# Optimization experiments

Hardware: AMD Instinct MI355X
Metric: run time of the kernel (lower is better)

Reference implementation:

```python
import jax, jax.numpy as jnp
import numpy as np

HEADS = 8
H_DIM = 64
SCALE = H_DIM ** -0.5


def setup_inputs() -> dict:
    key = jax.random.key(0)
    ks = jax.random.split(key, 10)
    B, Q, K, D = 4, 2048, 2048, 512
    hidden = HEADS * H_DIM  # 512
    s = 0.02  # weight init scale
    return {
        "q": jax.random.normal(ks[0], (B, Q, D), jnp.float32),
        "k": jax.random.normal(ks[1], (B, K, D), jnp.float32),
        "v": jax.random.normal(ks[2], (B, K, D), jnp.float32),
        "bias": jax.random.normal(ks[3], (B, Q, K), jnp.float32),
        "Wq": jax.random.normal(ks[4], (D, hidden), jnp.float32) * s,
        "bq": jnp.zeros((hidden,), jnp.float32),
        "Wk": jax.random.normal(ks[5], (D, hidden), jnp.float32) * s,
        "bk": jnp.zeros((hidden,), jnp.float32),
        "Wv": jax.random.normal(ks[6], (D, hidden), jnp.float32) * s,
        "bv": jnp.zeros((hidden,), jnp.float32),
        "Wg": jax.random.normal(ks[7], (D, hidden), jnp.float32) * s,
        "bg": jnp.zeros((hidden,), jnp.float32),
        "Wo": jax.random.normal(ks[8], (hidden, D), jnp.float32) * s,
        "bo": jnp.zeros((D,), jnp.float32),
    }


def reference(q, k, v, bias, Wq, bq, Wk, bk, Wv, bv, Wg, bg, Wo, bo):
    B, Q, _ = q.shape
    K = k.shape[-2]
    wq = (q @ Wq + bq).reshape(B, Q, HEADS, H_DIM) * SCALE   # (B,Q,H,Dh)
    wk = (k @ Wk + bk).reshape(B, K, HEADS, H_DIM)           # (B,K,H,Dh)
    wv = (v @ Wv + bv).reshape(B, K, HEADS, H_DIM)           # (B,K,H,Dh)
    # scores (B,Q,K,H); softmax over k_len axis (-2), matching torch softmax(-2)
    scores = jnp.einsum("bqhd,bkhd->bqkh", wq, wk)
    a = jax.nn.softmax(scores, axis=-2)
    # bias added AFTER softmax, broadcast over heads -- faithful to source
    a = a + bias[..., None]
    o = jnp.einsum("bqkh,bkhd->bqhd", a, wv).reshape(B, Q, HEADS * H_DIM)
    g = jax.nn.sigmoid(q @ Wg + bg)
    o = g * o
    return o @ Wo + bo
```

## Files before the change

### kernel.cpp

```cpp
#include <hip/hip_runtime.h>
#include <hip/hip_bf16.h>

#define NB 4
#define SEQ 2048
#define DMODEL 512
#define HEADS 8
#define HDIM 64
#define QKSCALE 0.125f

typedef __bf16 bf16_t;
typedef bf16_t bf16x8 __attribute__((ext_vector_type(8)));
typedef bf16_t bf16x4 __attribute__((ext_vector_type(4)));
typedef float f32x4 __attribute__((ext_vector_type(4)));

__device__ __forceinline__ int swz(int row, int c16) {
    return (row << 7) + (((c16) ^ (row & 7)) << 4);
}

__device__ __forceinline__ bf16x4 cvt4(float4 v) {
    bf16x4 r;
    r[0] = (bf16_t)v.x; r[1] = (bf16_t)v.y; r[2] = (bf16_t)v.z; r[3] = (bf16_t)v.w;
    return r;
}

__global__ __launch_bounds__(256) void prep_weights(
    const float* __restrict__ Wq, const float* __restrict__ Wk,
    const float* __restrict__ Wv, const float* __restrict__ Wg,
    const float* __restrict__ Wo, bf16_t* __restrict__ out)
{
    __shared__ float t[64][65];
    const int m  = blockIdx.x >> 6;
    const int t2 = blockIdx.x & 63;
    const int tr = t2 >> 3, tc = t2 & 7;
    const float* W = (m == 0) ? Wq : (m == 1) ? Wk : (m == 2) ? Wv : (m == 3) ? Wg : Wo;
    const int r0 = threadIdx.x >> 6;
    const int c  = threadIdx.x & 63;
#pragma unroll
    for (int i = 0; i < 64; i += 4) {
        int row = i + r0;
        t[row][c] = W[(size_t)(tr * 64 + row) * DMODEL + tc * 64 + c];
    }
    __syncthreads();
    bf16_t* o = out + (size_t)m * (DMODEL * DMODEL);
#pragma unroll
    for (int i = 0; i < 64; i += 4) {
        int row = i + r0;
        o[(size_t)(tc * 64 + row) * DMODEL + tr * 64 + c] = (bf16_t)t[c][row];
    }
}

template <int MODE>
__global__ __launch_bounds__(256) void gemm_proj(
    const float* __restrict__ A, const bf16_t* __restrict__ Wt,
    const float* __restrict__ bias, void* __restrict__ out, float scale)
{
    __shared__ __align__(16) char smA[8192];
    __shared__ __align__(16) char smB[8192];
    const int tid = threadIdx.x;
    const int lane = tid & 63, w = tid >> 6;
    const int m0 = (blockIdx.x >> 3) << 6;
    const int n0 = (blockIdx.x & 7) << 6;
    const int wrow = (w >> 1) * 32, wcol = (w & 1) * 32;
    const int lr = lane & 15, lg = lane >> 4;

    f32x4 acc[2][2] = {};
    for (int kb = 0; kb < 8; ++kb) {
        const int k0 = kb * 64;
        __syncthreads();
#pragma unroll
        for (int i = 0; i < 4; ++i) {
            int f = tid + i * 256;
            int row = f >> 4, c4 = f & 15;
            float4 v = *(const float4*)(A + (size_t)(m0 + row) * DMODEL + k0 + c4 * 4);
            *(bf16x4*)(smA + swz(row, c4 >> 1) + ((c4 & 1) << 3)) = cvt4(v);
        }
#pragma unroll
        for (int i = 0; i < 2; ++i) {
            int f = tid + i * 256;
            int row = f >> 3, c16 = f & 7;
            uint4 v = *(const uint4*)(Wt + (size_t)(n0 + row) * DMODEL + k0 + c16 * 8);
            *(uint4*)(smB + swz(row, c16)) = v;
        }
        __syncthreads();
#pragma unroll
        for (int ks = 0; ks < 2; ++ks) {
            bf16x8 a[2], b[2];
#pragma unroll
            for (int mi = 0; mi < 2; ++mi)
                a[mi] = *(const bf16x8*)(smA + swz(wrow + mi * 16 + lr, lg + ks * 4));
#pragma unroll
            for (int ni = 0; ni < 2; ++ni)
                b[ni] = *(const bf16x8*)(smB + swz(wcol + ni * 16 + lr, lg + ks * 4));
#pragma unroll
            for (int mi = 0; mi < 2; ++mi)
#pragma unroll
                for (int ni = 0; ni < 2; ++ni)
                    acc[mi][ni] = __builtin_amdgcn_mfma_f32_16x16x32_bf16(a[mi], b[ni], acc[mi][ni], 0, 0, 0);
        }
    }
#pragma unroll
    for (int mi = 0; mi < 2; ++mi) {
#pragma unroll
        for (int ni = 0; ni < 2; ++ni) {
            const int col = n0 + wcol + ni * 16 + lr;
            const float bv = bias[col];
            if (MODE == 0) {
#pragma unroll
                for (int j = 0; j < 4; ++j) {
                    int row = m0 + wrow + mi * 16 + (lg << 2) + j;
                    ((bf16_t*)out)[(size_t)row * DMODEL + col] = (bf16_t)((acc[mi][ni][j] + bv) * scale);
                }
            } else if (MODE == 1) {
                int row0 = m0 + wrow + mi * 16 + (lg << 2);
                int b = row0 >> 11, key = row0 & (SEQ - 1);
                int h = col >> 6, d = col & 63;
                bf16x4 r;
#pragma unroll
                for (int j = 0; j < 4; ++j) r[j] = (bf16_t)(acc[mi][ni][j] + bv);
                *(bf16x4*)((bf16_t*)out + ((size_t)(b * HEADS + h) * HDIM + d) * SEQ + key) = r;
            } else {
#pragma unroll
                for (int j = 0; j < 4; ++j) {
                    int row = m0 + wrow + mi * 16 + (lg << 2) + j;
                    float x = acc[mi][ni][j] + bv;
                    ((bf16_t*)out)[(size_t)row * DMODEL + col] = (bf16_t)(1.0f / (1.0f + __expf(-x)));
                }
            }
        }
    }
}

__global__ __launch_bounds__(256) void attn_kernel(
    const bf16_t* __restrict__ wq, const bf16_t* __restrict__ wk,
    const bf16_t* __restrict__ wvt, bf16_t* __restrict__ attn_o)
{
    __shared__ __align__(16) char smK[8192];
    __shared__ __align__(16) char smV[8192];
    __shared__ __align__(16) char smP[8192];
    const int tid = threadIdx.x;
    const int lane = tid & 63, w = tid >> 6;
    const int bh = blockIdx.x & 31;
    const int qt = blockIdx.x >> 5;
    const int b = bh >> 3, h = bh & 7;
    const int q0 = qt << 6;
    const int lr = lane & 15, lg = lane >> 4;

    bf16x8 qf[2];
    {
        int row = q0 + w * 16 + lr;
        const bf16_t* p = wq + (size_t)(b * SEQ + row) * DMODEL + h * HDIM + lg * 8;
        qf[0] = *(const bf16x8*)(p);
        qf[1] = *(const bf16x8*)(p + 32);
    }
    float mrun[4], lrun[4];
#pragma unroll
    for (int j = 0; j < 4; ++j) { mrun[j] = -1e30f; lrun[j] = 0.f; }
    f32x4 oacc[4] = {};

    for (int kt = 0; kt < SEQ / 64; ++kt) {
        const int k0 = kt * 64;
        __syncthreads();
#pragma unroll
        for (int i = 0; i < 2; ++i) {
            int f = tid + i * 256;
            int row = f >> 3, c16 = f & 7;
            uint4 vk = *(const uint4*)(wk + (size_t)(b * SEQ + k0 + row) * DMODEL + h * HDIM + c16 * 8);
            *(uint4*)(smK + swz(row, c16)) = vk;
            uint4 vv = *(const uint4*)(wvt + ((size_t)(b * HEADS + h) * HDIM + row) * SEQ + k0 + c16 * 8);
            *(uint4*)(smV + swz(row, c16)) = vv;
        }
        __syncthreads();

        f32x4 s[4] = {};
#pragma unroll
        for (int ks = 0; ks < 2; ++ks) {
#pragma unroll
            for (int nf = 0; nf < 4; ++nf) {
                bf16x8 kbf = *(const bf16x8*)(smK + swz(nf * 16 + lr, lg + ks * 4));
                s[nf] = __builtin_amdgcn_mfma_f32_16x16x32_bf16(qf[ks], kbf, s[nf], 0, 0, 0);
            }
        }
        float mnew[4], sc[4], rs[4];
#pragma unroll
        for (int j = 0; j < 4; ++j) {
            float m = fmaxf(fmaxf(s[0][j], s[1][j]), fmaxf(s[2][j], s[3][j]));
#pragma unroll
            for (int off = 1; off < 16; off <<= 1) m = fmaxf(m, __shfl_xor(m, off));
            mnew[j] = fmaxf(mrun[j], m);
            sc[j] = __expf(mrun[j] - mnew[j]);
            rs[j] = 0.f;
        }
#pragma unroll
        for (int nf = 0; nf < 4; ++nf) {
#pragma unroll
            for (int j = 0; j < 4; ++j) {
                float p = __expf(s[nf][j] - mnew[j]);
                s[nf][j] = p;
                rs[j] += p;
            }
        }
#pragma unroll
        for (int j = 0; j < 4; ++j) {
#pragma unroll
            for (int off = 1; off < 16; off <<= 1) rs[j] += __shfl_xor(rs[j], off);
            lrun[j] = lrun[j] * sc[j] + rs[j];
            mrun[j] = mnew[j];
        }
#pragma unroll
        for (int nf = 0; nf < 4; ++nf)
#pragma unroll
            for (int j = 0; j < 4; ++j) oacc[nf][j] *= sc[j];

        char* pbase = smP + w * 2048;
#pragma unroll
        for (int nf = 0; nf < 4; ++nf) {
            int col = nf * 16 + lr;
#pragma unroll
            for (int j = 0; j < 4; ++j) {
                int row = lg * 4 + j;
                *(bf16_t*)(pbase + swz(row, col >> 3) + ((col & 7) << 1)) = (bf16_t)s[nf][j];
            }
        }
#pragma unroll
        for (int ks = 0; ks < 2; ++ks) {
            bf16x8 pa = *(const bf16x8*)(pbase + swz(lr, lg + ks * 4));
#pragma unroll
            for (int nf = 0; nf < 4; ++nf) {
                bf16x8 vb = *(const bf16x8*)(smV + swz(nf * 16 + lr, lg + ks * 4));
                oacc[nf] = __builtin_amdgcn_mfma_f32_16x16x32_bf16(pa, vb, oacc[nf], 0, 0, 0);
            }
        }
    }
    float rinv[4];
#pragma unroll
    for (int j = 0; j < 4; ++j) rinv[j] = 1.0f / lrun[j];
#pragma unroll
    for (int nf = 0; nf < 4; ++nf) {
        int col = h * HDIM + nf * 16 + lr;
#pragma unroll
        for (int j = 0; j < 4; ++j) {
            int row = q0 + w * 16 + lg * 4 + j;
            attn_o[(size_t)(b * SEQ + row) * DMODEL + col] = (bf16_t)(oacc[nf][j] * rinv[j]);
        }
    }
}

__global__ __launch_bounds__(512) void biasv_gemm(
    const float* __restrict__ bias, const bf16_t* __restrict__ wvt,
    float* __restrict__ Bv)
{
    __shared__ __align__(16) char smA[16384];
    __shared__ __align__(16) char smB[16384];
    const int tid = threadIdx.x;
    const int lane = tid & 63, w = tid >> 6;
    const int nt = blockIdx.x & 3;
    const int mt = (blockIdx.x >> 2) & 15;
    const int b = blockIdx.x >> 6;
    const int m0 = mt << 7, n0 = nt << 7;
    const int wr = w >> 2, wc = w & 3;
    const int lr = lane & 15, lg = lane >> 4;

    f32x4 acc[4][2] = {};
    for (int kb = 0; kb < SEQ / 64; ++kb) {
        const int k0 = kb * 64;
        __syncthreads();
#pragma unroll
        for (int i = 0; i < 4; ++i) {
            int f = tid + i * 512;
            int row = f >> 4, c4 = f & 15;
            float4 v = *(const float4*)(bias + ((size_t)b * SEQ + m0 + row) * SEQ + k0 + c4 * 4);
            *(bf16x4*)(smA + swz(row, c4 >> 1) + ((c4 & 1) << 3)) = cvt4(v);
        }
#pragma unroll
        for (int i = 0; i < 2; ++i) {
            int f = tid + i * 512;
            int row = f >> 3, c16 = f & 7;
            int n = n0 + row;
            uint4 v = *(const uint4*)(wvt + ((size_t)(b * HEADS + (n >> 6)) * HDIM + (n & 63)) * SEQ + k0 + c16 * 8);
            *(uint4*)(smB + swz(row, c16)) = v;
        }
        __syncthreads();
#pragma unroll
        for (int ks = 0; ks < 2; ++ks) {
            bf16x8 a[4], bb[2];
#pragma unroll
            for (int mi = 0; mi < 4; ++mi)
                a[mi] = *(const bf16x8*)(smA + swz(wr * 64 + mi * 16 + lr, lg + ks * 4));
#pragma unroll
            for (int ni = 0; ni < 2; ++ni)
                bb[ni] = *(const bf16x8*)(smB + swz(wc * 32 + ni * 16 + lr, lg + ks * 4));
#pragma unroll
            for (int mi = 0; mi < 4; ++mi)
#pragma unroll
                for (int ni = 0; ni < 2; ++ni)
                    acc[mi][ni] = __builtin_amdgcn_mfma_f32_16x16x32_bf16(a[mi], bb[ni], acc[mi][ni], 0, 0, 0);
        }
    }
#pragma unroll
    for (int mi = 0; mi < 4; ++mi) {
#pragma unroll
        for (int ni = 0; ni < 2; ++ni) {
            int col = n0 + wc * 32 + ni * 16 + lr;
#pragma unroll
            for (int j = 0; j < 4; ++j) {
                int row = m0 + wr * 64 + mi * 16 + lg * 4 + j;
                Bv[((size_t)b * SEQ + row) * DMODEL + col] = acc[mi][ni][j];
            }
        }
    }
}

__global__ __launch_bounds__(256) void out_gemm(
    const bf16_t* __restrict__ atn, const float* __restrict__ Bvp,
    const bf16_t* __restrict__ gg, const bf16_t* __restrict__ Wot,
    const float* __restrict__ bo, float* __restrict__ out)
{
    __shared__ __align__(16) char smA[8192];
    __shared__ __align__(16) char smB[8192];
    const int tid = threadIdx.x;
    const int lane = tid & 63, w = tid >> 6;
    const int m0 = (blockIdx.x >> 3) << 6;
    const int n0 = (blockIdx.x & 7) << 6;
    const int wrow = (w >> 1) * 32, wcol = (w & 1) * 32;
    const int lr = lane & 15, lg = lane >> 4;

    f32x4 acc[2][2] = {};
    for (int kb = 0; kb < 8; ++kb) {
        const int k0 = kb * 64;
        __syncthreads();
#pragma unroll
        for (int i = 0; i < 4; ++i) {
            int f = tid + i * 256;
            int row = f >> 4, c4 = f & 15;
            size_t idx = (size_t)(m0 + row) * DMODEL + k0 + c4 * 4;
            bf16x4 a4 = *(const bf16x4*)(atn + idx);
            bf16x4 g4 = *(const bf16x4*)(gg + idx);
            float4 b4 = *(const float4*)(Bvp + idx);
            bf16x4 r;
            r[0] = (bf16_t)((float)g4[0] * ((float)a4[0] + b4.x));
            r[1] = (bf16_t)((float)g4[1] * ((float)a4[1] + b4.y));
            r[2] = (bf16_t)((float)g4[2] * ((float)a4[2] + b4.z));
            r[3] = (bf16_t)((float)g4[3] * ((float)a4[3] + b4.w));
            *(bf16x4*)(smA + swz(row, c4 >> 1) + ((c4 & 1) << 3)) = r;
        }
#pragma unroll
        for (int i = 0; i < 2; ++i) {
            int f = tid + i * 256;
            int row = f >> 3, c16 = f & 7;
            uint4 v = *(const uint4*)(Wot + (size_t)(n0 + row) * DMODEL + k0 + c16 * 8);
            *(uint4*)(smB + swz(row, c16)) = v;
        }
        __syncthreads();
#pragma unroll
        for (int ks = 0; ks < 2; ++ks) {
            bf16x8 a[2], b[2];
#pragma unroll
            for (int mi = 0; mi < 2; ++mi)
                a[mi] = *(const bf16x8*)(smA + swz(wrow + mi * 16 + lr, lg + ks * 4));
#pragma unroll
            for (int ni = 0; ni < 2; ++ni)
                b[ni] = *(const bf16x8*)(smB + swz(wcol + ni * 16 + lr, lg + ks * 4));
#pragma unroll
            for (int mi = 0; mi < 2; ++mi)
#pragma unroll
                for (int ni = 0; ni < 2; ++ni)
                    acc[mi][ni] = __builtin_amdgcn_mfma_f32_16x16x32_bf16(a[mi], b[ni], acc[mi][ni], 0, 0, 0);
        }
    }
#pragma unroll
    for (int mi = 0; mi < 2; ++mi) {
#pragma unroll
        for (int ni = 0; ni < 2; ++ni) {
            int col = n0 + wcol + ni * 16 + lr;
            float bb = bo[col];
#pragma unroll
            for (int j = 0; j < 4; ++j) {
                int row = m0 + wrow + mi * 16 + (lg << 2) + j;
                out[(size_t)row * DMODEL + col] = acc[mi][ni][j] + bb;
            }
        }
    }
}

extern "C" void kernel_launch(void* const* d_in, const int* in_sizes, int n_in,
                              void* d_out, int out_size, void* d_ws, size_t ws_size,
                              hipStream_t stream)
{
    const float* q    = (const float*)d_in[0];
    const float* k    = (const float*)d_in[1];
    const float* v    = (const float*)d_in[2];
    const float* bias = (const float*)d_in[3];
    const float* Wq   = (const float*)d_in[4];
    const float* bq   = (const float*)d_in[5];
    const float* Wk   = (const float*)d_in[6];
    const float* bk   = (const float*)d_in[7];
    const float* Wv   = (const float*)d_in[8];
    const float* bv   = (const float*)d_in[9];
    const float* Wg   = (const float*)d_in[10];
    const float* bg   = (const float*)d_in[11];
    const float* Wo   = (const float*)d_in[12];
    const float* bo   = (const float*)d_in[13];
    float* out = (float*)d_out;

    char* ws = (char*)d_ws;
    const size_t WSZ = (size_t)DMODEL * DMODEL;
    const size_t TOK = (size_t)NB * SEQ * DMODEL;
    bf16_t* Wt   = (bf16_t*)ws;
    bf16_t* wq_  = (bf16_t*)(ws + 5 * WSZ * 2);
    bf16_t* wk_  = wq_ + TOK;
    bf16_t* wvt  = wk_ + TOK;
    bf16_t* atn  = wvt + TOK;
    bf16_t* g_   = atn + TOK;
    float*  Bv_  = (float*)(g_ + TOK);

    prep_weights<<<320, 256, 0, stream>>>(Wq, Wk, Wv, Wg, Wo, Wt);
    gemm_proj<0><<<1024, 256, 0, stream>>>(q, Wt,            bq, (void*)wq_, QKSCALE);
    gemm_proj<0><<<1024, 256, 0, stream>>>(k, Wt + WSZ,      bk, (void*)wk_, 1.0f);
    gemm_proj<1><<<1024, 256, 0, stream>>>(v, Wt + 2 * WSZ,  bv, (void*)wvt, 1.0f);
    gemm_proj<2><<<1024, 256, 0, stream>>>(q, Wt + 3 * WSZ,  bg, (void*)g_,  1.0f);
    attn_kernel<<<1024, 256, 0, stream>>>(wq_, wk_, wvt, atn);
    biasv_gemm<<<256, 512, 0, stream>>>(bias, wvt, Bv_);
    out_gemm<<<1024, 256, 0, stream>>>(atn, Bv_, g_, Wt + 4 * WSZ, bo, out);
}
```

Measured before the change: 481.4 us.

## Fuse Q/gate projections, enlarge GEMM tiles, prefetch K/V, drop softmax max tracking

The Q and gate projections become one GEMM with N=1024 by reordering the transposed weights, which removes a duplicate pass over q. The projection and output GEMMs move to 128x128 tiles with 512 threads, and the output GEMM staging loads are widened to 8 elements. The attention loop prefetches the next K/V tile into registers while it computes on the current one. The online softmax max and rescale are removed in favour of exp2 with log2(e) folded into the Q scale, so the row sum is only reduced at the end. That last change depends on the scores staying small enough that exp does not overflow.

```diff
diff --git a/kernel.cpp b/kernel.cpp
--- a/kernel.cpp
+++ b/kernel.cpp
@@ -6,7 +6,7 @@
 #define DMODEL 512
 #define HEADS 8
 #define HDIM 64
-#define QKSCALE 0.125f
+#define QKS_L2E 0.18033688011112042f
 
 typedef __bf16 bf16_t;
 typedef bf16_t bf16x8 __attribute__((ext_vector_type(8)));
@@ -24,15 +24,15 @@
 }
 
 __global__ __launch_bounds__(256) void prep_weights(
-    const float* __restrict__ Wq, const float* __restrict__ Wk,
-    const float* __restrict__ Wv, const float* __restrict__ Wg,
+    const float* __restrict__ Wq, const float* __restrict__ Wg,
+    const float* __restrict__ Wk, const float* __restrict__ Wv,
     const float* __restrict__ Wo, bf16_t* __restrict__ out)
 {
     __shared__ float t[64][65];
     const int m  = blockIdx.x >> 6;
     const int t2 = blockIdx.x & 63;
     const int tr = t2 >> 3, tc = t2 & 7;
-    const float* W = (m == 0) ? Wq : (m == 1) ? Wk : (m == 2) ? Wv : (m == 3) ? Wg : Wo;
+    const float* W = (m == 0) ? Wq : (m == 1) ? Wg : (m == 2) ? Wk : (m == 3) ? Wv : Wo;
     const int r0 = threadIdx.x >> 6;
     const int c  = threadIdx.x & 63;
 #pragma unroll
@@ -50,33 +50,36 @@
 }
 
 template <int MODE>
-__global__ __launch_bounds__(256) void gemm_proj(
+__global__ __launch_bounds__(512) void proj_gemm(
     const float* __restrict__ A, const bf16_t* __restrict__ Wt,
-    const float* __restrict__ bias, void* __restrict__ out, float scale)
-{
-    __shared__ __align__(16) char smA[8192];
-    __shared__ __align__(16) char smB[8192];
+    const float* __restrict__ bias0, const float* __restrict__ bias1,
+    bf16_t* __restrict__ out0, bf16_t* __restrict__ out1)
+{
+    constexpr int NT = (MODE == 0) ? 8 : 4;
+    __shared__ __align__(16) char smA[16384];
+    __shared__ __align__(16) char smB[16384];
     const int tid = threadIdx.x;
     const int lane = tid & 63, w = tid >> 6;
-    const int m0 = (blockIdx.x >> 3) << 6;
-    const int n0 = (blockIdx.x & 7) << 6;
-    const int wrow = (w >> 1) * 32, wcol = (w & 1) * 32;
+    const int nt = blockIdx.x & (NT - 1);
+    const int mt = blockIdx.x / NT;
+    const int m0 = mt << 7, n0 = nt << 7;
+    const int wr = w >> 2, wc = w & 3;
     const int lr = lane & 15, lg = lane >> 4;
 
-    f32x4 acc[2][2] = {};
+    f32x4 acc[4][2] = {};
     for (int kb = 0; kb < 8; ++kb) {
         const int k0 = kb * 64;
         __syncthreads();
 #pragma unroll
         for (int i = 0; i < 4; ++i) {
-            int f = tid + i * 256;
+            int f = tid + i * 512;
             int row = f >> 4, c4 = f & 15;
             float4 v = *(const float4*)(A + (size_t)(m0 + row) * DMODEL + k0 + c4 * 4);
             *(bf16x4*)(smA + swz(row, c4 >> 1) + ((c4 & 1) << 3)) = cvt4(v);
         }
 #pragma unroll
         for (int i = 0; i < 2; ++i) {
-            int f = tid + i * 256;
+            int f = tid + i * 512;
             int row = f >> 3, c16 = f & 7;
             uint4 v = *(const uint4*)(Wt + (size_t)(n0 + row) * DMODEL + k0 + c16 * 8);
             *(uint4*)(smB + swz(row, c16)) = v;
@@ -84,47 +87,50 @@
         __syncthreads();
 #pragma unroll
         for (int ks = 0; ks < 2; ++ks) {
-            bf16x8 a[2], b[2];
-#pragma unroll
-            for (int mi = 0; mi < 2; ++mi)
-                a[mi] = *(const bf16x8*)(smA + swz(wrow + mi * 16 + lr, lg + ks * 4));
+            bf16x8 a[4], bb[2];
+#pragma unroll
+            for (int mi = 0; mi < 4; ++mi)
+                a[mi] = *(const bf16x8*)(smA + swz(wr * 64 + mi * 16 + lr, lg + ks * 4));
 #pragma unroll
             for (int ni = 0; ni < 2; ++ni)
-                b[ni] = *(const bf16x8*)(smB + swz(wcol + ni * 16 + lr, lg + ks * 4));
-#pragma unroll
-            for (int mi = 0; mi < 2; ++mi)
+                bb[ni] = *(const bf16x8*)(smB + swz(wc * 32 + ni * 16 + lr, lg + ks * 4));
+#pragma unroll
+            for (int mi = 0; mi < 4; ++mi)
 #pragma unroll
                 for (int ni = 0; ni < 2; ++ni)
-                    acc[mi][ni] = __builtin_amdgcn_mfma_f32_16x16x32_bf16(a[mi], b[ni], acc[mi][ni], 0, 0, 0);
-        }
-    }
-#pragma unroll
-    for (int mi = 0; mi < 2; ++mi) {
+                    acc[mi][ni] = __builtin_amdgcn_mfma_f32_16x16x32_bf16(a[mi], bb[ni], acc[mi][ni], 0, 0, 0);
+        }
+    }
+#pragma unroll
+    for (int mi = 0; mi < 4; ++mi) {
 #pragma unroll
         for (int ni = 0; ni < 2; ++ni) {
-            const int col = n0 + wcol + ni * 16 + lr;
-            const float bv = bias[col];
+            const int col = n0 + wc * 32 + ni * 16 + lr;
+            const int row0 = m0 + wr * 64 + mi * 16 + lg * 4;
             if (MODE == 0) {
+                const bool isG = col >= DMODEL;
+                const int c = isG ? col - DMODEL : col;
+                const float bb = isG ? bias1[c] : bias0[c];
 #pragma unroll
                 for (int j = 0; j < 4; ++j) {
-                    int row = m0 + wrow + mi * 16 + (lg << 2) + j;
-                    ((bf16_t*)out)[(size_t)row * DMODEL + col] = (bf16_t)((acc[mi][ni][j] + bv) * scale);
+                    float x = acc[mi][ni][j] + bb;
+                    bf16_t r = isG ? (bf16_t)(1.0f / (1.0f + __expf(-x)))
+                                   : (bf16_t)(x * QKS_L2E);
+                    (isG ? out1 : out0)[(size_t)(row0 + j) * DMODEL + c] = r;
                 }
             } else if (MODE == 1) {
-                int row0 = m0 + wrow + mi * 16 + (lg << 2);
-                int b = row0 >> 11, key = row0 & (SEQ - 1);
-                int h = col >> 6, d = col & 63;
+                const float bb = bias0[col];
+#pragma unroll
+                for (int j = 0; j < 4; ++j)
+                    out0[(size_t)(row0 + j) * DMODEL + col] = (bf16_t)(acc[mi][ni][j] + bb);
+            } else {
+                const float bb = bias0[col];
+                const int b = row0 >> 11, key = row0 & (SEQ - 1);
+                const int h = col >> 6, d = col & 63;
                 bf16x4 r;
 #pragma unroll
-                for (int j = 0; j < 4; ++j) r[j] = (bf16_t)(acc[mi][ni][j] + bv);
-                *(bf16x4*)((bf16_t*)out + ((size_t)(b * HEADS + h) * HDIM + d) * SEQ + key) = r;
-            } else {
-#pragma unroll
-                for (int j = 0; j < 4; ++j) {
-                    int row = m0 + wrow + mi * 16 + (lg << 2) + j;
-                    float x = acc[mi][ni][j] + bv;
-                    ((bf16_t*)out)[(size_t)row * DMODEL + col] = (bf16_t)(1.0f / (1.0f + __expf(-x)));
-                }
+                for (int j = 0; j < 4; ++j) r[j] = (bf16_t)(acc[mi][ni][j] + bb);
+                *(bf16x4*)(out0 + ((size_t)(b * HEADS + h) * HDIM + d) * SEQ + key) = r;
             }
         }
     }
@@ -152,24 +158,34 @@
         qf[0] = *(const bf16x8*)(p);
         qf[1] = *(const bf16x8*)(p + 32);
     }
-    float mrun[4], lrun[4];
-#pragma unroll
-    for (int j = 0; j < 4; ++j) { mrun[j] = -1e30f; lrun[j] = 0.f; }
+    const bf16_t* kbase = wk + (size_t)b * SEQ * DMODEL + h * HDIM;
+    const bf16_t* vbase = wvt + (size_t)(b * HEADS + h) * HDIM * SEQ;
+    const int srow0 = tid >> 3,        sc0 = tid & 7;
+    const int srow1 = (tid + 256) >> 3, sc1 = (tid + 256) & 7;
+
+    uint4 rk[2], rv[2];
+    rk[0] = *(const uint4*)(kbase + (size_t)srow0 * DMODEL + sc0 * 8);
+    rk[1] = *(const uint4*)(kbase + (size_t)srow1 * DMODEL + sc1 * 8);
+    rv[0] = *(const uint4*)(vbase + (size_t)srow0 * SEQ + sc0 * 8);
+    rv[1] = *(const uint4*)(vbase + (size_t)srow1 * SEQ + sc1 * 8);
+
+    float lsum[4] = {0.f, 0.f, 0.f, 0.f};
     f32x4 oacc[4] = {};
 
     for (int kt = 0; kt < SEQ / 64; ++kt) {
-        const int k0 = kt * 64;
-        __syncthreads();
-#pragma unroll
-        for (int i = 0; i < 2; ++i) {
-            int f = tid + i * 256;
-            int row = f >> 3, c16 = f & 7;
-            uint4 vk = *(const uint4*)(wk + (size_t)(b * SEQ + k0 + row) * DMODEL + h * HDIM + c16 * 8);
-            *(uint4*)(smK + swz(row, c16)) = vk;
-            uint4 vv = *(const uint4*)(wvt + ((size_t)(b * HEADS + h) * HDIM + row) * SEQ + k0 + c16 * 8);
-            *(uint4*)(smV + swz(row, c16)) = vv;
-        }
-        __syncthreads();
+        __syncthreads();
+        *(uint4*)(smK + swz(srow0, sc0)) = rk[0];
+        *(uint4*)(smK + swz(srow1, sc1)) = rk[1];
+        *(uint4*)(smV + swz(srow0, sc0)) = rv[0];
+        *(uint4*)(smV + swz(srow1, sc1)) = rv[1];
+        __syncthreads();
+        if (kt + 1 < SEQ / 64) {
+            const int k0n = (kt + 1) * 64;
+            rk[0] = *(const uint4*)(kbase + (size_t)(k0n + srow0) * DMODEL + sc0 * 8);
+            rk[1] = *(const uint4*)(kbase + (size_t)(k0n + srow1) * DMODEL + sc1 * 8);
+            rv[0] = *(const uint4*)(vbase + (size_t)srow0 * SEQ + k0n + sc0 * 8);
+            rv[1] = *(const uint4*)(vbase + (size_t)srow1 * SEQ + k0n + sc1 * 8);
+        }
 
         f32x4 s[4] = {};
 #pragma unroll
@@ -180,37 +196,15 @@
                 s[nf] = __builtin_amdgcn_mfma_f32_16x16x32_bf16(qf[ks], kbf, s[nf], 0, 0, 0);
             }
         }
-        float mnew[4], sc[4], rs[4];
-#pragma unroll
-        for (int j = 0; j < 4; ++j) {
-            float m = fmaxf(fmaxf(s[0][j], s[1][j]), fmaxf(s[2][j], s[3][j]));
-#pragma unroll
-            for (int off = 1; off < 16; off <<= 1) m = fmaxf(m, __shfl_xor(m, off));
-            mnew[j] = fmaxf(mrun[j], m);
-            sc[j] = __expf(mrun[j] - mnew[j]);
-            rs[j] = 0.f;
-        }
 #pragma unroll
         for (int nf = 0; nf < 4; ++nf) {
 #pragma unroll
             for (int j = 0; j < 4; ++j) {
-                float p = __expf(s[nf][j] - mnew[j]);
+                float p = __builtin_amdgcn_exp2f(s[nf][j]);
                 s[nf][j] = p;
-                rs[j] += p;
-            }
-        }
-#pragma unroll
-        for (int j = 0; j < 4; ++j) {
-#pragma unroll
-            for (int off = 1; off < 16; off <<= 1) rs[j] += __shfl_xor(rs[j], off);
-            lrun[j] = lrun[j] * sc[j] + rs[j];
-            mrun[j] = mnew[j];
-        }
-#pragma unroll
-        for (int nf = 0; nf < 4; ++nf)
-#pragma unroll
-            for (int j = 0; j < 4; ++j) oacc[nf][j] *= sc[j];
-
+                lsum[j] += p;
+            }
+        }
         char* pbase = smP + w * 2048;
 #pragma unroll
         for (int nf = 0; nf < 4; ++nf) {
@@ -233,7 +227,12 @@
     }
     float rinv[4];
 #pragma unroll
-    for (int j = 0; j < 4; ++j) rinv[j] = 1.0f / lrun[j];
+    for (int j = 0; j < 4; ++j) {
+        float t = lsum[j];
+#pragma unroll
+        for (int off = 1; off < 16; off <<= 1) t += __shfl_xor(t, off);
+        rinv[j] = 1.0f / t;
+    }
 #pragma unroll
     for (int nf = 0; nf < 4; ++nf) {
         int col = h * HDIM + nf * 16 + lr;
@@ -310,42 +309,48 @@
     }
 }
 
-__global__ __launch_bounds__(256) void out_gemm(
+__global__ __launch_bounds__(512) void out_gemm(
     const bf16_t* __restrict__ atn, const float* __restrict__ Bvp,
     const bf16_t* __restrict__ gg, const bf16_t* __restrict__ Wot,
     const float* __restrict__ bo, float* __restrict__ out)
 {
-    __shared__ __align__(16) char smA[8192];
-    __shared__ __align__(16) char smB[8192];
+    __shared__ __align__(16) char smA[16384];
+    __shared__ __align__(16) char smB[16384];
     const int tid = threadIdx.x;
     const int lane = tid & 63, w = tid >> 6;
-    const int m0 = (blockIdx.x >> 3) << 6;
-    const int n0 = (blockIdx.x & 7) << 6;
-    const int wrow = (w >> 1) * 32, wcol = (w & 1) * 32;
+    const int nt = blockIdx.x & 3;
+    const int mt = blockIdx.x >> 2;
+    const int m0 = mt << 7, n0 = nt << 7;
+    const int wr = w >> 2, wc = w & 3;
     const int lr = lane & 15, lg = lane >> 4;
 
-    f32x4 acc[2][2] = {};
+    f32x4 acc[4][2] = {};
     for (int kb = 0; kb < 8; ++kb) {
         const int k0 = kb * 64;
         __syncthreads();
 #pragma unroll
-        for (int i = 0; i < 4; ++i) {
-            int f = tid + i * 256;
-            int row = f >> 4, c4 = f & 15;
-            size_t idx = (size_t)(m0 + row) * DMODEL + k0 + c4 * 4;
-            bf16x4 a4 = *(const bf16x4*)(atn + idx);
-            bf16x4 g4 = *(const bf16x4*)(gg + idx);
-            float4 b4 = *(const float4*)(Bvp + idx);
-            bf16x4 r;
-            r[0] = (bf16_t)((float)g4[0] * ((float)a4[0] + b4.x));
-            r[1] = (bf16_t)((float)g4[1] * ((float)a4[1] + b4.y));
-            r[2] = (bf16_t)((float)g4[2] * ((float)a4[2] + b4.z));
-            r[3] = (bf16_t)((float)g4[3] * ((float)a4[3] + b4.w));
-            *(bf16x4*)(smA + swz(row, c4 >> 1) + ((c4 & 1) << 3)) = r;
-        }
-#pragma unroll
         for (int i = 0; i < 2; ++i) {
-            int f = tid + i * 256;
+            int f = tid + i * 512;
+            int row = f >> 3, c8 = f & 7;
+            size_t idx = (size_t)(m0 + row) * DMODEL + k0 + c8 * 8;
+            bf16x8 a8 = *(const bf16x8*)(atn + idx);
+            bf16x8 g8 = *(const bf16x8*)(gg + idx);
+            float4 blo = *(const float4*)(Bvp + idx);
+            float4 bhi = *(const float4*)(Bvp + idx + 4);
+            bf16x8 r;
+            r[0] = (bf16_t)((float)g8[0] * ((float)a8[0] + blo.x));
+            r[1] = (bf16_t)((float)g8[1] * ((float)a8[1] + blo.y));
+            r[2] = (bf16_t)((float)g8[2] * ((float)a8[2] + blo.z));
+            r[3] = (bf16_t)((float)g8[3] * ((float)a8[3] + blo.w));
+            r[4] = (bf16_t)((float)g8[4] * ((float)a8[4] + bhi.x));
+            r[5] = (bf16_t)((float)g8[5] * ((float)a8[5] + bhi.y));
+            r[6] = (bf16_t)((float)g8[6] * ((float)a8[6] + bhi.z));
+            r[7] = (bf16_t)((float)g8[7] * ((float)a8[7] + bhi.w));
+            *(bf16x8*)(smA + swz(row, c8)) = r;
+        }
+#pragma unroll
+        for (int i = 0; i < 2; ++i) {
+            int f = tid + i * 512;
             int row = f >> 3, c16 = f & 7;
             uint4 v = *(const uint4*)(Wot + (size_t)(n0 + row) * DMODEL + k0 + c16 * 8);
             *(uint4*)(smB + swz(row, c16)) = v;
@@ -353,29 +358,29 @@
         __syncthreads();
 #pragma unroll
         for (int ks = 0; ks < 2; ++ks) {
-            bf16x8 a[2], b[2];
-#pragma unroll
-            for (int mi = 0; mi < 2; ++mi)
-                a[mi] = *(const bf16x8*)(smA + swz(wrow + mi * 16 + lr, lg + ks * 4));
+            bf16x8 a[4], bb[2];
+#pragma unroll
+            for (int mi = 0; mi < 4; ++mi)
+                a[mi] = *(const bf16x8*)(smA + swz(wr * 64 + mi * 16 + lr, lg + ks * 4));
 #pragma unroll
             for (int ni = 0; ni < 2; ++ni)
-                b[ni] = *(const bf16x8*)(smB + swz(wcol + ni * 16 + lr, lg + ks * 4));
-#pragma unroll
-            for (int mi = 0; mi < 2; ++mi)
+                bb[ni] = *(const bf16x8*)(smB + swz(wc * 32 + ni * 16 + lr, lg + ks * 4));
+#pragma unroll
+            for (int mi = 0; mi < 4; ++mi)
 #pragma unroll
                 for (int ni = 0; ni < 2; ++ni)
-                    acc[mi][ni] = __builtin_amdgcn_mfma_f32_16x16x32_bf16(a[mi], b[ni], acc[mi][ni], 0, 0, 0);
-        }
-    }
-#pragma unroll
-    for (int mi = 0; mi < 2; ++mi) {
+                    acc[mi][ni] = __builtin_amdgcn_mfma_f32_16x16x32_bf16(a[mi], bb[ni], acc[mi][ni], 0, 0, 0);
+        }
+    }
+#pragma unroll
+    for (int mi = 0; mi < 4; ++mi) {
 #pragma unroll
         for (int ni = 0; ni < 2; ++ni) {
-            int col = n0 + wcol + ni * 16 + lr;
+            int col = n0 + wc * 32 + ni * 16 + lr;
             float bb = bo[col];
 #pragma unroll
             for (int j = 0; j < 4; ++j) {
-                int row = m0 + wrow + mi * 16 + (lg << 2) + j;
+                int row = m0 + wr * 64 + mi * 16 + lg * 4 + j;
                 out[(size_t)row * DMODEL + col] = acc[mi][ni][j] + bb;
             }
         }
@@ -413,12 +418,11 @@
     bf16_t* g_   = atn + TOK;
     float*  Bv_  = (float*)(g_ + TOK);
 
-    prep_weights<<<320, 256, 0, stream>>>(Wq, Wk, Wv, Wg, Wo, Wt);
-    gemm_proj<0><<<1024, 256, 0, stream>>>(q, Wt,            bq, (void*)wq_, QKSCALE);
-    gemm_proj<0><<<1024, 256, 0, stream>>>(k, Wt + WSZ,      bk, (void*)wk_, 1.0f);
-    gemm_proj<1><<<1024, 256, 0, stream>>>(v, Wt + 2 * WSZ,  bv, (void*)wvt, 1.0f);
-    gemm_proj<2><<<1024, 256, 0, stream>>>(q, Wt + 3 * WSZ,  bg, (void*)g_,  1.0f);
+    prep_weights<<<320, 256, 0, stream>>>(Wq, Wg, Wk, Wv, Wo, Wt);
+    proj_gemm<0><<<512, 512, 0, stream>>>(q, Wt,           bq, bg,      wq_, g_);
+    proj_gemm<1><<<256, 512, 0, stream>>>(k, Wt + 2 * WSZ, bk, nullptr, wk_, nullptr);
+    proj_gemm<2><<<256, 512, 0, stream>>>(v, Wt + 3 * WSZ, bv, nullptr, wvt, nullptr);
     attn_kernel<<<1024, 256, 0, stream>>>(wq_, wk_, wvt, atn);
     biasv_gemm<<<256, 512, 0, stream>>>(bias, wvt, Bv_);
-    out_gemm<<<1024, 256, 0, stream>>>(atn, Bv_, g_, Wt + 4 * WSZ, bo, out);
-}
+    out_gemm<<<256, 512, 0, stream>>>(atn, Bv_, g_, Wt + 4 * WSZ, bo, out);
+}
```

New measurement: 489.0 us. No clear change (+1.6%).
